# Optimization experiments

Measured on AMD Instinct MI355X. Metric: run time of the kernel, lower is better.

## Reference

```python
import jax, jax.numpy as jnp
import numpy as np

N = 100000   # nodes
E = 1600000  # edges
HID = 128    # hidden_dim
H = 8        # heads
C = HID // H # head_dim = out_channels per head


def setup_inputs() -> dict:
    key = jax.random.key(0)
    ks = jax.random.split(key, 10)
    x = jax.random.normal(ks[0], (N, HID), jnp.float32)
    edge_index = jax.random.randint(ks[1], (2, E), 0, N, dtype=jnp.int64)
    edge_attr = jax.random.uniform(ks[2], (E,), jnp.float32)
    # GATConv params (lin_src == lin_dst shared since in_channels is int)
    W = jax.random.normal(ks[3], (HID, H * C), jnp.float32) / np.sqrt(HID)
    att_src = jax.random.normal(ks[4], (H, C), jnp.float32) / np.sqrt(C)
    att_dst = jax.random.normal(ks[5], (H, C), jnp.float32) / np.sqrt(C)
    # lin_edge: Linear(edge_dim=1, H*C, bias=False) -> weight [H*C, 1] stored as [H, C]
    w_edge = jax.random.normal(ks[6], (H, C), jnp.float32)
    att_edge = jax.random.normal(ks[7], (H, C), jnp.float32) / np.sqrt(C)
    bias = jnp.zeros((H * C,), jnp.float32)
    gamma = jnp.ones((HID,), jnp.float32)
    beta = jnp.zeros((HID,), jnp.float32)
    return dict(x=x, edge_index=edge_index, edge_attr=edge_attr, W=W,
                att_src=att_src, att_dst=att_dst, w_edge=w_edge,
                att_edge=att_edge, bias=bias, gamma=gamma, beta=beta)


def reference(x, edge_index, edge_attr, W, att_src, att_dst, w_edge, att_edge, bias, gamma, beta):
    n = x.shape[0]
    src, dst = edge_index[0], edge_index[1]
    # add_self_loops with fill_value='mean': loop edge_attr = per-dst-node mean of edge_attr
    ones = jnp.ones_like(edge_attr)
    deg = jax.ops.segment_sum(ones, dst, num_segments=n)
    loop_attr = jax.ops.segment_sum(edge_attr, dst, num_segments=n) / jnp.maximum(deg, 1.0)
    ar = jnp.arange(n, dtype=src.dtype)
    src = jnp.concatenate([src, ar])
    dst = jnp.concatenate([dst, ar])
    ea = jnp.concatenate([edge_attr, loop_attr])  # [E+N]

    h = (x @ W).reshape(n, H, C)                  # [N,H,C]
    a_src = (h * att_src).sum(-1)                 # [N,H]
    a_dst = (h * att_dst).sum(-1)                 # [N,H]
    # edge_dim=1: alpha_edge = <lin_edge(ea), att_edge> = ea * sum(w_edge*att_edge)
    w_e = (w_edge * att_edge).sum(-1)             # [H]
    alpha = a_src[src] + a_dst[dst] + ea[:, None] * w_e  # [E+N, H]
    alpha = jax.nn.leaky_relu(alpha, 0.2)
    # segment softmax over incoming edges of each dst node (all nodes have a self-loop)
    m = jax.ops.segment_max(alpha, dst, num_segments=n)      # [N,H]
    ex = jnp.exp(alpha - m[dst])
    denom = jax.ops.segment_sum(ex, dst, num_segments=n)     # [N,H]
    p = ex / (denom[dst] + 1e-16)
    # scatter-aggregate weighted messages, concat heads, bias
    out = jax.ops.segment_sum(p[:, :, None] * h[src], dst, num_segments=n)
    out = out.reshape(n, H * C) + bias
    # residual + LayerNorm + ReLU
    y = out + x
    mu = y.mean(-1, keepdims=True)
    var = ((y - mu) ** 2).mean(-1, keepdims=True)
    y = (y - mu) * jax.lax.rsqrt(var + 1e-5) * gamma + beta
    return jax.nn.relu(y)
```

## Files before the change

### kernel.cpp

```cpp
#include <hip/hip_runtime.h>
#include <math.h>

#define HID 128
#define HEADS 8
#define CDIM 16
#define NB1 256

typedef short bf8 __attribute__((ext_vector_type(8)));
typedef float f32x4 __attribute__((ext_vector_type(4)));

__device__ __forceinline__ unsigned short f2bf(float f) {
    unsigned u = __float_as_uint(f);
    unsigned r = (u + 0x7fffu + ((u >> 16) & 1u)) >> 16;
    return (unsigned short)r;
}
__device__ __forceinline__ float bf2f(unsigned short u) {
    return __uint_as_float(((unsigned)u) << 16);
}

__global__ __launch_bounds__(256) void k_tw(const float* __restrict__ W,
                                            unsigned short* __restrict__ Wt) {
    int idx = blockIdx.x * 256 + threadIdx.x;
    int j = idx >> 7, k = idx & 127;
    Wt[idx] = f2bf(W[k * HID + j]);
}

__global__ __launch_bounds__(256) void k_hist(const int* __restrict__ dst,
                                              int* __restrict__ cntmat,
                                              int E, int per, int nbkt) {
    __shared__ int h[256];
    int t = threadIdx.x;
    h[t] = 0;
    __syncthreads();
    int b0 = blockIdx.x * per;
    int b1 = min(b0 + per, E);
    for (int e = b0 + t; e < b1; e += 256)
        atomicAdd(&h[dst[e] >> 9], 1);
    __syncthreads();
    if (t < nbkt) cntmat[t * NB1 + blockIdx.x] = h[t];
}

__global__ __launch_bounds__(256) void kscanA(const int* __restrict__ in,
                                              int* __restrict__ tmp,
                                              int* __restrict__ bsum, int M) {
    __shared__ int lds[256];
    int t = threadIdx.x;
    int base = blockIdx.x * 1024 + t * 4;
    int v[4];
#pragma unroll
    for (int i = 0; i < 4; i++) {
        int idx = base + i;
        v[i] = (idx < M) ? in[idx] : 0;
    }
    int s = v[0] + v[1] + v[2] + v[3];
    lds[t] = s;
    __syncthreads();
    for (int off = 1; off < 256; off <<= 1) {
        int xv = (t >= off) ? lds[t - off] : 0;
        __syncthreads();
        lds[t] += xv;
        __syncthreads();
    }
    int run = (t > 0) ? lds[t - 1] : 0;
#pragma unroll
    for (int i = 0; i < 4; i++) {
        int idx = base + i;
        if (idx < M) tmp[idx] = run;
        run += v[i];
    }
    if (t == 255) bsum[blockIdx.x] = lds[255];
}

__global__ __launch_bounds__(128) void kscanB(const int* __restrict__ bsum,
                                              int* __restrict__ bscan, int nb,
                                              const float* __restrict__ w_edge,
                                              const float* __restrict__ att_edge,
                                              float* __restrict__ w_e) {
    __shared__ int lds[128];
    int t = threadIdx.x;
    if (t < HEADS) {
        float s = 0.f;
        for (int c = 0; c < CDIM; c++) s += w_edge[t * CDIM + c] * att_edge[t * CDIM + c];
        w_e[t] = s;
    }
    lds[t] = (t < nb) ? bsum[t] : 0;
    __syncthreads();
    for (int off = 1; off < 128; off <<= 1) {
        int xv = (t >= off) ? lds[t - off] : 0;
        __syncthreads();
        lds[t] += xv;
        __syncthreads();
    }
    bscan[t] = (t > 0) ? lds[t - 1] : 0;
}

__global__ __launch_bounds__(256) void k_scat(const int* __restrict__ src,
                                              const int* __restrict__ dst,
                                              const float* __restrict__ eattr,
                                              const int* __restrict__ tmp,
                                              const int* __restrict__ bscan,
                                              int* __restrict__ d1,
                                              int2* __restrict__ erec1,
                                              int E, int per, int nbkt) {
    __shared__ int cur[256];
    int t = threadIdx.x;
    if (t < nbkt) {
        int idx = t * NB1 + blockIdx.x;
        cur[t] = tmp[idx] + bscan[idx >> 10];
    }
    __syncthreads();
    int b0 = blockIdx.x * per;
    int b1 = min(b0 + per, E);
    for (int e = b0 + t; e < b1; e += 256) {
        int d = dst[e];
        int pos = atomicAdd(&cur[d >> 9], 1);
        d1[pos] = d;
        erec1[pos] = make_int2(src[e], __float_as_int(eattr[e]));
    }
}

__global__ __launch_bounds__(256) void k_bin(const int* __restrict__ tmp,
                                             const int* __restrict__ bscan,
                                             const int* __restrict__ d1,
                                             const int2* __restrict__ erec1,
                                             int* __restrict__ row_ptr,
                                             int2* __restrict__ erec,
                                             int N, int E, int nbkt) {
    __shared__ int h2[512];
    __shared__ int s2[256];
    __shared__ int cur2[512];
    int b = blockIdx.x, t = threadIdx.x;
    int i0 = b * NB1;
    int base = tmp[i0] + bscan[i0 >> 10];
    int end = E;
    if (b + 1 < nbkt) {
        int i1 = (b + 1) * NB1;
        end = tmp[i1] + bscan[i1 >> 10];
    }
    h2[t] = 0; h2[t + 256] = 0;
    __syncthreads();
    for (int e = base + t; e < end; e += 256)
        atomicAdd(&h2[d1[e] & 511], 1);
    __syncthreads();
    int a0 = h2[2 * t], a1 = h2[2 * t + 1];
    s2[t] = a0 + a1;
    __syncthreads();
    for (int off = 1; off < 256; off <<= 1) {
        int v = (t >= off) ? s2[t - off] : 0;
        __syncthreads();
        s2[t] += v;
        __syncthreads();
    }
    int ex = (t > 0) ? s2[t - 1] : 0;
    int p0 = base + ex;
    int p1 = p0 + a0;
    int ng = b * 512 + 2 * t;
    if (ng <= N) row_ptr[ng] = p0;
    if (ng + 1 <= N) row_ptr[ng + 1] = p1;
    cur2[2 * t] = p0;
    cur2[2 * t + 1] = p1;
    __syncthreads();
    for (int e = base + t; e < end; e += 256) {
        int d = d1[e];
        int pos = atomicAdd(&cur2[d & 511], 1);
        erec[pos] = erec1[e];
    }
}

__global__ __launch_bounds__(256) void k_gemm(const float* __restrict__ x,
                                              const unsigned short* __restrict__ Wt,
                                              const float* __restrict__ att_src,
                                              const float* __restrict__ att_dst,
                                              unsigned short* __restrict__ hbf,
                                              float* __restrict__ a_src,
                                              float* __restrict__ a_dst, int N) {
    int tid = threadIdx.x;
    int wv = tid >> 6, lane = tid & 63;
    int nloc = lane & 15, q = lane >> 4;
    int node = blockIdx.x * 64 + wv * 16 + nloc;
    int nc = min(node, N - 1);
    const float* xp = x + (size_t)nc * HID + q * 8;
    const unsigned short* wp = Wt + nloc * HID + q * 8;
    f32x4 acc[8];
#pragma unroll
    for (int i = 0; i < 8; i++) acc[i] = (f32x4){0.f, 0.f, 0.f, 0.f};
#pragma unroll
    for (int ch = 0; ch < 4; ch++) {
        float4 xv0 = *(const float4*)(xp + ch * 32);
        float4 xv1 = *(const float4*)(xp + ch * 32 + 4);
        bf8 bfrag;
        bfrag[0] = (short)f2bf(xv0.x); bfrag[1] = (short)f2bf(xv0.y);
        bfrag[2] = (short)f2bf(xv0.z); bfrag[3] = (short)f2bf(xv0.w);
        bfrag[4] = (short)f2bf(xv1.x); bfrag[5] = (short)f2bf(xv1.y);
        bfrag[6] = (short)f2bf(xv1.z); bfrag[7] = (short)f2bf(xv1.w);
#pragma unroll
        for (int jt = 0; jt < 8; jt++) {
            bf8 afrag = *(const bf8*)(wp + (size_t)jt * 16 * HID + ch * 32);
            acc[jt] = __builtin_amdgcn_mfma_f32_16x16x32_bf16(afrag, bfrag, acc[jt], 0, 0, 0);
        }
    }
    bool ok = node < N;
    size_t hb = (size_t)nc * HID;
#pragma unroll
    for (int jt = 0; jt < 8; jt++) {
        int j0 = jt * 16 + q * 4;
        float4 as4 = *(const float4*)(att_src + j0);
        float4 ad4 = *(const float4*)(att_dst + j0);
        f32x4 a = acc[jt];
        float ps = a[0] * as4.x + a[1] * as4.y + a[2] * as4.z + a[3] * as4.w;
        float pd = a[0] * ad4.x + a[1] * ad4.y + a[2] * ad4.z + a[3] * ad4.w;
        ps += __shfl_xor(ps, 16, 64); ps += __shfl_xor(ps, 32, 64);
        pd += __shfl_xor(pd, 16, 64); pd += __shfl_xor(pd, 32, 64);
        if (ok) {
            ushort4 hv;
            hv.x = f2bf(a[0]); hv.y = f2bf(a[1]); hv.z = f2bf(a[2]); hv.w = f2bf(a[3]);
            *(ushort4*)(hbf + hb + j0) = hv;
            if (q == 0) {
                a_src[(size_t)node * 8 + jt] = ps;
                a_dst[(size_t)node * 8 + jt] = pd;
            }
        }
    }
}

__global__ __launch_bounds__(256) void k_node(const int* __restrict__ row_ptr,
                                              const int2* __restrict__ erec,
                                              const float* __restrict__ a_src,
                                              const float* __restrict__ a_dst,
                                              const float* __restrict__ w_e,
                                              const unsigned short* __restrict__ hbf,
                                              const float* __restrict__ x,
                                              const float* __restrict__ bias,
                                              const float* __restrict__ gamma,
                                              const float* __restrict__ beta,
                                              float* __restrict__ out, int N) {
    int wv = threadIdx.x >> 6;
    int lane = threadIdx.x & 63;
    int n = blockIdx.x * 4 + wv;
    if (n >= N) return;
    int r0 = row_ptr[n], r1 = row_ptr[n + 1];
    int sub = lane >> 4;
    int colg = lane & 15;
    int wh = colg >> 1;
    float ad_h = a_dst[(size_t)n * 8 + wh];
    float we_h = w_e[wh];

    float acc[8];
#pragma unroll
    for (int j = 0; j < 8; j++) acc[j] = 0.f;
    float wsum = 0.f, suma = 0.f;

    int e = r0 + sub;
    if (e < r1) {
        int2 rec = erec[e];
        for (;;) {
            int en = e + 4;
            bool more = (en < r1);
            int2 recn;
            if (more) recn = erec[en];
            int s = rec.x;
            float a = __int_as_float(rec.y);
            const unsigned short* hp = hbf + (size_t)s * HID + colg * 8;
            bf8 hv = *(const bf8*)hp;
            float asv = a_src[(size_t)s * 8 + wh];
            float v = asv + ad_h + a * we_h;
            v = v > 0.f ? v : 0.2f * v;
            float w = __expf(v);
            wsum += w;
            suma += (colg == 0) ? a : 0.f;
#pragma unroll
            for (int j = 0; j < 8; j++)
                acc[j] = fmaf(w, bf2f((unsigned short)hv[j]), acc[j]);
            if (!more) break;
            e = en;
            rec = recn;
        }
    }

#pragma unroll
    for (int j = 0; j < 8; j++) {
        acc[j] += __shfl_xor(acc[j], 16, 64);
        acc[j] += __shfl_xor(acc[j], 32, 64);
    }
    wsum += __shfl_xor(wsum, 16, 64);
    wsum += __shfl_xor(wsum, 32, 64);
    suma += __shfl_xor(suma, 16, 64);
    suma += __shfl_xor(suma, 32, 64);

    float accA = sub == 0 ? acc[0] : sub == 1 ? acc[2] : sub == 2 ? acc[4] : acc[6];
    float accB = sub == 0 ? acc[1] : sub == 1 ? acc[3] : sub == 2 ? acc[5] : acc[7];
    int srcL = ((lane & 3) << 4) | (lane >> 2);
    float a0 = __shfl(accA, srcL, 64);
    float a1 = __shfl(accB, srcL, 64);
    int head = lane >> 3;
    float denom = __shfl(wsum, head << 1, 64);
    float sa = __shfl(suma, 0, 64);

    int deg = r1 - r0;
    float la = sa / fmaxf((float)deg, 1.0f);
    float adh = a_dst[(size_t)n * 8 + head];
    float weh = w_e[head];
    float vs = a_src[(size_t)n * 8 + head] + adh + la * weh;
    vs = vs > 0.f ? vs : 0.2f * vs;
    float exs = __expf(vs);
    size_t bx = (size_t)n * HID;
    ushort2 hs = *(const ushort2*)(hbf + bx + 2 * lane);
    a0 = fmaf(exs, bf2f(hs.x), a0);
    a1 = fmaf(exs, bf2f(hs.y), a1);
    float inv = 1.f / (denom + exs + 1e-16f);

    float2 xv = *(const float2*)(x + bx + 2 * lane);
    float2 bv = *(const float2*)(bias + 2 * lane);
    float y0 = a0 * inv + bv.x + xv.x;
    float y1 = a1 * inv + bv.y + xv.y;
    float ss = y0 + y1, sq = y0 * y0 + y1 * y1;
#pragma unroll
    for (int off = 32; off; off >>= 1) {
        ss += __shfl_xor(ss, off, 64);
        sq += __shfl_xor(sq, off, 64);
    }
    float mu = ss * (1.f / 128.f);
    float var = sq * (1.f / 128.f) - mu * mu;
    float r = rsqrtf(fmaxf(var, 0.f) + 1e-5f);
    float2 gv = *(const float2*)(gamma + 2 * lane);
    float2 tv = *(const float2*)(beta + 2 * lane);
    float o0 = (y0 - mu) * r * gv.x + tv.x;
    float o1 = (y1 - mu) * r * gv.y + tv.y;
    float2 ov = make_float2(fmaxf(o0, 0.f), fmaxf(o1, 0.f));
    *(float2*)(out + bx + 2 * lane) = ov;
}

extern "C" void kernel_launch(void* const* d_in, const int* in_sizes, int n_in,
                              void* d_out, int out_size, void* d_ws, size_t ws_size,
                              hipStream_t stream) {
    const float* x        = (const float*)d_in[0];
    const int*   ei       = (const int*)d_in[1];
    const float* eattr    = (const float*)d_in[2];
    const float* W        = (const float*)d_in[3];
    const float* att_src  = (const float*)d_in[4];
    const float* att_dst  = (const float*)d_in[5];
    const float* w_edge   = (const float*)d_in[6];
    const float* att_edge = (const float*)d_in[7];
    const float* bias     = (const float*)d_in[8];
    const float* gamma    = (const float*)d_in[9];
    const float* beta     = (const float*)d_in[10];

    int N = in_sizes[0] / HID;
    int E = in_sizes[2];
    const int* src = ei;
    const int* dst = ei + E;
    float* out = (float*)d_out;

    int nbkt = (N + 511) >> 9;
    int M = nbkt * NB1;
    int per = (E + NB1 - 1) / NB1;

    char* ws = (char*)d_ws;
    size_t off = 0;
    auto alloc = [&](size_t bytes) { char* p = ws + off; off += (bytes + 255) & ~255ull; return p; };
    unsigned short* hbf = (unsigned short*)alloc((size_t)N * HID * 2);
    unsigned short* Wt  = (unsigned short*)alloc((size_t)HID * HID * 2);
    float* a_src   = (float*)alloc((size_t)N * 8 * 4);
    float* a_dst   = (float*)alloc((size_t)N * 8 * 4);
    int2*  erec    = (int2*) alloc((size_t)E * 8);
    int2*  erec1   = (int2*) alloc((size_t)E * 8);
    int*   d1      = (int*)  alloc((size_t)E * 4);
    int*   cntmat  = (int*)  alloc((size_t)M * 4);
    int*   stmp    = (int*)  alloc((size_t)M * 4);
    int*   bsum    = (int*)  alloc(128 * 4);
    int*   bscan   = (int*)  alloc(128 * 4);
    int*   row_ptr = (int*)  alloc((size_t)(N + 1) * 4);
    float* w_e     = (float*)alloc(8 * 4);

    int nbA = (M + 1023) / 1024;

    k_tw<<<64, 256, 0, stream>>>(W, Wt);
    k_hist<<<NB1, 256, 0, stream>>>(dst, cntmat, E, per, nbkt);
    kscanA<<<nbA, 256, 0, stream>>>(cntmat, stmp, bsum, M);
    kscanB<<<1, 128, 0, stream>>>(bsum, bscan, nbA, w_edge, att_edge, w_e);
    k_scat<<<NB1, 256, 0, stream>>>(src, dst, eattr, stmp, bscan, d1, erec1, E, per, nbkt);
    k_bin<<<nbkt, 256, 0, stream>>>(stmp, bscan, d1, erec1, row_ptr, erec, N, E, nbkt);
    k_gemm<<<(N + 63) / 64, 256, 0, stream>>>(x, Wt, att_src, att_dst, hbf, a_src, a_dst, N);
    k_node<<<(N + 3) / 4, 256, 0, stream>>>(row_ptr, erec, a_src, a_dst, w_e, hbf, x,
                                            bias, gamma, beta, out, N);
}
```

Before: 335.3 us.

## Replace two-level bucket sort with atomic degree count and direct CSR scatter

```diff
diff --git a/kernel.cpp b/kernel.cpp
--- a/kernel.cpp
+++ b/kernel.cpp
@@ -4,7 +4,6 @@
 #define HID 128
 #define HEADS 8
 #define CDIM 16
-#define NB1 256
 
 typedef short bf8 __attribute__((ext_vector_type(8)));
 typedef float f32x4 __attribute__((ext_vector_type(4)));
@@ -19,25 +18,21 @@
 }
 
 __global__ __launch_bounds__(256) void k_tw(const float* __restrict__ W,
-                                            unsigned short* __restrict__ Wt) {
+                                            unsigned short* __restrict__ Wt,
+                                            int* __restrict__ deg, int N) {
     int idx = blockIdx.x * 256 + threadIdx.x;
-    int j = idx >> 7, k = idx & 127;
-    Wt[idx] = f2bf(W[k * HID + j]);
-}
-
-__global__ __launch_bounds__(256) void k_hist(const int* __restrict__ dst,
-                                              int* __restrict__ cntmat,
-                                              int E, int per, int nbkt) {
-    __shared__ int h[256];
-    int t = threadIdx.x;
-    h[t] = 0;
-    __syncthreads();
-    int b0 = blockIdx.x * per;
-    int b1 = min(b0 + per, E);
-    for (int e = b0 + t; e < b1; e += 256)
-        atomicAdd(&h[dst[e] >> 9], 1);
-    __syncthreads();
-    if (t < nbkt) cntmat[t * NB1 + blockIdx.x] = h[t];
+    if (idx < HID * HID) {
+        int j = idx >> 7, k = idx & 127;
+        Wt[idx] = f2bf(W[k * HID + j]);
+    }
+    if (idx < N) deg[idx] = 0;
+}
+
+__global__ __launch_bounds__(256) void k_deg(const int* __restrict__ dst,
+                                             int* __restrict__ deg, int E) {
+    int i = blockIdx.x * 256 + threadIdx.x;
+    int stride = gridDim.x * 256;
+    for (int e = i; e < E; e += stride) atomicAdd(&deg[dst[e]], 1);
 }
 
 __global__ __launch_bounds__(256) void kscanA(const int* __restrict__ in,
@@ -94,86 +89,34 @@
     bscan[t] = (t > 0) ? lds[t - 1] : 0;
 }
 
-__global__ __launch_bounds__(256) void k_scat(const int* __restrict__ src,
-                                              const int* __restrict__ dst,
-                                              const float* __restrict__ eattr,
-                                              const int* __restrict__ tmp,
-                                              const int* __restrict__ bscan,
-                                              int* __restrict__ d1,
-                                              int2* __restrict__ erec1,
-                                              int E, int per, int nbkt) {
-    __shared__ int cur[256];
-    int t = threadIdx.x;
-    if (t < nbkt) {
-        int idx = t * NB1 + blockIdx.x;
-        cur[t] = tmp[idx] + bscan[idx >> 10];
-    }
-    __syncthreads();
-    int b0 = blockIdx.x * per;
-    int b1 = min(b0 + per, E);
-    for (int e = b0 + t; e < b1; e += 256) {
-        int d = dst[e];
-        int pos = atomicAdd(&cur[d >> 9], 1);
-        d1[pos] = d;
-        erec1[pos] = make_int2(src[e], __float_as_int(eattr[e]));
-    }
-}
-
-__global__ __launch_bounds__(256) void k_bin(const int* __restrict__ tmp,
+__global__ __launch_bounds__(256) void k_mid(const float* __restrict__ x,
+                                             const unsigned short* __restrict__ Wt,
+                                             const float* __restrict__ att_src,
+                                             const float* __restrict__ att_dst,
+                                             unsigned short* __restrict__ hbf,
+                                             float* __restrict__ a_src,
+                                             float* __restrict__ a_dst,
+                                             const int* __restrict__ src,
+                                             const int* __restrict__ dst,
+                                             const float* __restrict__ eattr,
+                                             const int* __restrict__ tmp,
                                              const int* __restrict__ bscan,
-                                             const int* __restrict__ d1,
-                                             const int2* __restrict__ erec1,
-                                             int* __restrict__ row_ptr,
+                                             int* __restrict__ deg,
                                              int2* __restrict__ erec,
-                                             int N, int E, int nbkt) {
-    __shared__ int h2[512];
-    __shared__ int s2[256];
-    __shared__ int cur2[512];
-    int b = blockIdx.x, t = threadIdx.x;
-    int i0 = b * NB1;
-    int base = tmp[i0] + bscan[i0 >> 10];
-    int end = E;
-    if (b + 1 < nbkt) {
-        int i1 = (b + 1) * NB1;
-        end = tmp[i1] + bscan[i1 >> 10];
-    }
-    h2[t] = 0; h2[t + 256] = 0;
-    __syncthreads();
-    for (int e = base + t; e < end; e += 256)
-        atomicAdd(&h2[d1[e] & 511], 1);
-    __syncthreads();
-    int a0 = h2[2 * t], a1 = h2[2 * t + 1];
-    s2[t] = a0 + a1;
-    __syncthreads();
-    for (int off = 1; off < 256; off <<= 1) {
-        int v = (t >= off) ? s2[t - off] : 0;
-        __syncthreads();
-        s2[t] += v;
-        __syncthreads();
-    }
-    int ex = (t > 0) ? s2[t - 1] : 0;
-    int p0 = base + ex;
-    int p1 = p0 + a0;
-    int ng = b * 512 + 2 * t;
-    if (ng <= N) row_ptr[ng] = p0;
-    if (ng + 1 <= N) row_ptr[ng + 1] = p1;
-    cur2[2 * t] = p0;
-    cur2[2 * t + 1] = p1;
-    __syncthreads();
-    for (int e = base + t; e < end; e += 256) {
-        int d = d1[e];
-        int pos = atomicAdd(&cur2[d & 511], 1);
-        erec[pos] = erec1[e];
-    }
-}
-
-__global__ __launch_bounds__(256) void k_gemm(const float* __restrict__ x,
-                                              const unsigned short* __restrict__ Wt,
-                                              const float* __restrict__ att_src,
-                                              const float* __restrict__ att_dst,
-                                              unsigned short* __restrict__ hbf,
-                                              float* __restrict__ a_src,
-                                              float* __restrict__ a_dst, int N) {
+                                             int N, int E, int gemmBlocks,
+                                             int scatBlocks) {
+    if ((int)blockIdx.x >= gemmBlocks) {
+        int bid = blockIdx.x - gemmBlocks;
+        int i = bid * 256 + threadIdx.x;
+        int stride = scatBlocks * 256;
+        for (int e = i; e < E; e += stride) {
+            int d = dst[e];
+            int old = atomicAdd(&deg[d], -1);
+            int pos = tmp[d] + bscan[d >> 10] + old - 1;
+            erec[pos] = make_int2(src[e], __float_as_int(eattr[e]));
+        }
+        return;
+    }
     int tid = threadIdx.x;
     int wv = tid >> 6, lane = tid & 63;
     int nloc = lane & 15, q = lane >> 4;
@@ -223,7 +166,8 @@
     }
 }
 
-__global__ __launch_bounds__(256) void k_node(const int* __restrict__ row_ptr,
+__global__ __launch_bounds__(512) void k_node(const int* __restrict__ tmp,
+                                              const int* __restrict__ bscan,
                                               const int2* __restrict__ erec,
                                               const float* __restrict__ a_src,
                                               const float* __restrict__ a_dst,
@@ -233,12 +177,13 @@
                                               const float* __restrict__ bias,
                                               const float* __restrict__ gamma,
                                               const float* __restrict__ beta,
-                                              float* __restrict__ out, int N) {
+                                              float* __restrict__ out, int N, int E) {
     int wv = threadIdx.x >> 6;
     int lane = threadIdx.x & 63;
-    int n = blockIdx.x * 4 + wv;
+    int n = blockIdx.x * 8 + wv;
     if (n >= N) return;
-    int r0 = row_ptr[n], r1 = row_ptr[n + 1];
+    int r0 = tmp[n] + bscan[n >> 10];
+    int r1 = (n + 1 < N) ? (tmp[n + 1] + bscan[(n + 1) >> 10]) : E;
     int sub = lane >> 4;
     int colg = lane & 15;
     int wh = colg >> 1;
@@ -250,30 +195,29 @@
     for (int j = 0; j < 8; j++) acc[j] = 0.f;
     float wsum = 0.f, suma = 0.f;
 
-    int e = r0 + sub;
-    if (e < r1) {
-        int2 rec = erec[e];
-        for (;;) {
-            int en = e + 4;
-            bool more = (en < r1);
-            int2 recn;
-            if (more) recn = erec[en];
-            int s = rec.x;
-            float a = __int_as_float(rec.y);
-            const unsigned short* hp = hbf + (size_t)s * HID + colg * 8;
-            bf8 hv = *(const bf8*)hp;
-            float asv = a_src[(size_t)s * 8 + wh];
-            float v = asv + ad_h + a * we_h;
-            v = v > 0.f ? v : 0.2f * v;
-            float w = __expf(v);
-            wsum += w;
-            suma += (colg == 0) ? a : 0.f;
-#pragma unroll
-            for (int j = 0; j < 8; j++)
-                acc[j] = fmaf(w, bf2f((unsigned short)hv[j]), acc[j]);
-            if (!more) break;
-            e = en;
-            rec = recn;
+    for (int e = r0 + (sub << 1); e < r1; e += 8) {
+        int2 rec0 = erec[e];
+        bool m1 = (e + 1) < r1;
+        int2 rec1 = m1 ? erec[e + 1] : rec0;
+        int s0 = rec0.x, s1 = rec1.x;
+        float ae0 = __int_as_float(rec0.y);
+        float ae1 = __int_as_float(rec1.y);
+        bf8 hv0 = *(const bf8*)(hbf + (size_t)s0 * HID + colg * 8);
+        bf8 hv1 = *(const bf8*)(hbf + (size_t)s1 * HID + colg * 8);
+        float as0 = a_src[(size_t)s0 * 8 + wh];
+        float as1 = a_src[(size_t)s1 * 8 + wh];
+        float v0 = as0 + ad_h + ae0 * we_h;
+        float v1 = as1 + ad_h + ae1 * we_h;
+        v0 = v0 > 0.f ? v0 : 0.2f * v0;
+        v1 = v1 > 0.f ? v1 : 0.2f * v1;
+        float w0 = __expf(v0);
+        float w1 = m1 ? __expf(v1) : 0.f;
+        wsum += w0 + w1;
+        if (colg == 0) suma += ae0 + (m1 ? ae1 : 0.f);
+#pragma unroll
+        for (int j = 0; j < 8; j++) {
+            acc[j] = fmaf(w0, bf2f((unsigned short)hv0[j]), acc[j]);
+            acc[j] = fmaf(w1, bf2f((unsigned short)hv1[j]), acc[j]);
         }
     }
 
@@ -351,10 +295,6 @@
     const int* dst = ei + E;
     float* out = (float*)d_out;
 
-    int nbkt = (N + 511) >> 9;
-    int M = nbkt * NB1;
-    int per = (E + NB1 - 1) / NB1;
-
     char* ws = (char*)d_ws;
     size_t off = 0;
     auto alloc = [&](size_t bytes) { char* p = ws + off; off += (bytes + 255) & ~255ull; return p; };
@@ -363,24 +303,23 @@
     float* a_src   = (float*)alloc((size_t)N * 8 * 4);
     float* a_dst   = (float*)alloc((size_t)N * 8 * 4);
     int2*  erec    = (int2*) alloc((size_t)E * 8);
-    int2*  erec1   = (int2*) alloc((size_t)E * 8);
-    int*   d1      = (int*)  alloc((size_t)E * 4);
-    int*   cntmat  = (int*)  alloc((size_t)M * 4);
-    int*   stmp    = (int*)  alloc((size_t)M * 4);
+    int*   deg     = (int*)  alloc((size_t)N * 4);
+    int*   tmp     = (int*)  alloc((size_t)N * 4);
     int*   bsum    = (int*)  alloc(128 * 4);
     int*   bscan   = (int*)  alloc(128 * 4);
-    int*   row_ptr = (int*)  alloc((size_t)(N + 1) * 4);
     float* w_e     = (float*)alloc(8 * 4);
 
-    int nbA = (M + 1023) / 1024;
-
-    k_tw<<<64, 256, 0, stream>>>(W, Wt);
-    k_hist<<<NB1, 256, 0, stream>>>(dst, cntmat, E, per, nbkt);
-    kscanA<<<nbA, 256, 0, stream>>>(cntmat, stmp, bsum, M);
+    int nbA = (N + 1023) / 1024;
+    int gemmBlocks = (N + 63) / 64;
+    int scatBlocks = 1024;
+
+    k_tw<<<512, 256, 0, stream>>>(W, Wt, deg, N);
+    k_deg<<<2048, 256, 0, stream>>>(dst, deg, E);
+    kscanA<<<nbA, 256, 0, stream>>>(deg, tmp, bsum, N);
     kscanB<<<1, 128, 0, stream>>>(bsum, bscan, nbA, w_edge, att_edge, w_e);
-    k_scat<<<NB1, 256, 0, stream>>>(src, dst, eattr, stmp, bscan, d1, erec1, E, per, nbkt);
-    k_bin<<<nbkt, 256, 0, stream>>>(stmp, bscan, d1, erec1, row_ptr, erec, N, E, nbkt);
-    k_gemm<<<(N + 63) / 64, 256, 0, stream>>>(x, Wt, att_src, att_dst, hbf, a_src, a_dst, N);
-    k_node<<<(N + 3) / 4, 256, 0, stream>>>(row_ptr, erec, a_src, a_dst, w_e, hbf, x,
-                                            bias, gamma, beta, out, N);
-}
+    k_mid<<<gemmBlocks + scatBlocks, 256, 0, stream>>>(
+        x, Wt, att_src, att_dst, hbf, a_src, a_dst,
+        src, dst, eattr, tmp, bscan, deg, erec, N, E, gemmBlocks, scatBlocks);
+    k_node<<<(N + 7) / 8, 512, 0, stream>>>(tmp, bscan, erec, a_src, a_dst, w_e, hbf, x,
+                                            bias, gamma, beta, out, N, E);
+}
```

Result: slower. 401.7 us (+19.8%).
